# Performance work log

Hardware: AMD Instinct MI355X
Metric: run time of the kernel (lower is better)

## Reference

```python
import jax, jax.numpy as jnp
import numpy as np

B, IN, OUT, E = 4096, 256, 256, 16


def setup_inputs() -> dict:
    key = jax.random.key(0)
    k1, k2, k3, k4, k5, k6 = jax.random.split(key, 6)
    return {
        "input": jax.random.normal(k1, (B, IN), dtype=jnp.float32),
        "route_index": jax.random.randint(k2, (B,), 0, E),
        "weight": jax.random.normal(k3, (E, OUT * IN), dtype=jnp.float32) * 0.02,
        "weight_fact": jax.random.normal(k4, (1, OUT * IN), dtype=jnp.float32) * 0.02,
        "bias": jax.random.normal(k5, (E, OUT), dtype=jnp.float32) * 0.02,
        "bias_fact": jax.random.normal(k6, (1, OUT), dtype=jnp.float32) * 0.02,
    }


def reference(input, route_index, weight, weight_fact, bias, bias_fact):
    b = input.shape[0]
    # per-token expert weight gather + shared factorized weight
    expert_weight = (weight[route_index] + weight_fact).reshape(b, OUT, IN)
    expert_bias = bias[route_index] + bias_fact  # [b, OUT]
    # batched matvec
    out = jnp.einsum("bmn,bn->bm", expert_weight, input) + expert_bias
    return out
```

## Files before the change

### kernel.cpp

```cpp
#include <hip/hip_runtime.h>


#define B_TOK 4096
#define IN_F 256
#define OUT_F 256
#define NEXP 16
#define WEL (OUT_F * IN_F)
#define NSB 16

typedef __attribute__((ext_vector_type(8))) short bhalf8;
typedef __attribute__((ext_vector_type(4))) float v4f;

#define WSUM_OFF 0u
#define PART_OFF 2097152u

__device__ __forceinline__ unsigned short f2bf(float f) {
    unsigned u = __float_as_uint(f);
    u += 0x7FFFu + ((u >> 16) & 1u);
    return (unsigned short)(u >> 16);
}

__global__ __launch_bounds__(256) void k_prep(
    const int* __restrict__ ridx, const float* __restrict__ w,
    const float* __restrict__ wf, unsigned short* __restrict__ wsum,
    int* __restrict__ part) {
    int bid = blockIdx.x;
    int tid = threadIdx.x;
    if (bid < 512) {
        int id = (bid * 256 + tid) * 8;
        const float4 a0 = *(const float4*)(w + id);
        const float4 a1 = *(const float4*)(w + id + 4);
        int fo = id & (WEL - 1);
        const float4 f0 = *(const float4*)(wf + fo);
        const float4 f1 = *(const float4*)(wf + fo + 4);
        bhalf8 v;
        v[0] = (short)f2bf(a0.x + f0.x); v[1] = (short)f2bf(a0.y + f0.y);
        v[2] = (short)f2bf(a0.z + f0.z); v[3] = (short)f2bf(a0.w + f0.w);
        v[4] = (short)f2bf(a1.x + f1.x); v[5] = (short)f2bf(a1.y + f1.y);
        v[6] = (short)f2bf(a1.z + f1.z); v[7] = (short)f2bf(a1.w + f1.w);
        *(bhalf8*)(wsum + id) = v;
    } else {
        __shared__ int h[NEXP];
        if (tid < NEXP) h[tid] = 0;
        __syncthreads();
        int sb = bid - 512;
        atomicAdd(&h[ridx[sb * 256 + tid]], 1);
        __syncthreads();
        if (tid < NEXP) part[sb * NEXP + tid] = h[tid];
    }
}

__global__ __launch_bounds__(256) void k_gemm(
    const unsigned short* __restrict__ wsum, const float* __restrict__ x,
    const int* __restrict__ ridx, const int* __restrict__ part,
    const float* __restrict__ bias, const float* __restrict__ bf,
    float* __restrict__ out) {
    __shared__ int pfx[NSB + 1];
    __shared__ int wc[4];
    __shared__ int stk[16];

    int e = blockIdx.y;
    int j = blockIdx.x;
    int tid = threadIdx.x;

    __shared__ int pc[NSB];
    if (tid < NSB) pc[tid] = part[tid * NEXP + e];
    __syncthreads();
    if (tid == 0) {
        int a = 0;
        for (int sb = 0; sb < NSB; ++sb) { pfx[sb] = a; a += pc[sb]; }
        pfx[NSB] = a;
    }
    __syncthreads();
    int cnt = pfx[NSB];
    int start = j * 16;
    if (start >= cnt) return;
    int rem = cnt - start;
    int rows = rem < 16 ? rem : 16;
    int end = start + rows;

    int wave = tid >> 6;
    int lane = tid & 63;

    for (int sb = 0; sb < NSB; ++sb) {
        if (pfx[sb + 1] <= start || pfx[sb] >= end) continue;
        int tok = sb * 256 + tid;
        bool m = (ridx[tok] == e);
        unsigned long long mask = __ballot(m);
        if (lane == 0) wc[wave] = (int)__popcll(mask);
        __syncthreads();
        int wbase = 0;
        for (int wv = 0; wv < wave; ++wv) wbase += wc[wv];
        int rank = wbase + (int)__popcll(mask & ((1ull << lane) - 1ull));
        int slot = pfx[sb] + rank;
        if (m && slot >= start && slot < end) stk[slot - start] = tok;
        __syncthreads();
    }
    if (tid < 16 && tid >= rows) stk[tid] = stk[0];
    __syncthreads();

    int l15 = lane & 15;
    int quad = lane >> 4;

    const float* xrow = x + stk[l15] * IN_F + quad * 8;
    const unsigned short* wbase_p =
        wsum + e * WEL + (wave * 64 + l15) * IN_F + quad * 8;

    v4f acc[4];
    #pragma unroll
    for (int n = 0; n < 4; ++n) acc[n] = (v4f){0.f, 0.f, 0.f, 0.f};

    #pragma unroll
    for (int ks = 0; ks < 8; ++ks) {
        const float4 a0 = *(const float4*)(xrow + ks * 32);
        const float4 a1 = *(const float4*)(xrow + ks * 32 + 4);
        bhalf8 a;
        a[0] = (short)f2bf(a0.x); a[1] = (short)f2bf(a0.y);
        a[2] = (short)f2bf(a0.z); a[3] = (short)f2bf(a0.w);
        a[4] = (short)f2bf(a1.x); a[5] = (short)f2bf(a1.y);
        a[6] = (short)f2bf(a1.z); a[7] = (short)f2bf(a1.w);
        bhalf8 b0 = *(const bhalf8*)(wbase_p + 0 * 16 * IN_F + ks * 32);
        bhalf8 b1 = *(const bhalf8*)(wbase_p + 1 * 16 * IN_F + ks * 32);
        bhalf8 b2 = *(const bhalf8*)(wbase_p + 2 * 16 * IN_F + ks * 32);
        bhalf8 b3 = *(const bhalf8*)(wbase_p + 3 * 16 * IN_F + ks * 32);
        acc[0] = __builtin_amdgcn_mfma_f32_16x16x32_bf16(a, b0, acc[0], 0, 0, 0);
        acc[1] = __builtin_amdgcn_mfma_f32_16x16x32_bf16(a, b1, acc[1], 0, 0, 0);
        acc[2] = __builtin_amdgcn_mfma_f32_16x16x32_bf16(a, b2, acc[2], 0, 0, 0);
        acc[3] = __builtin_amdgcn_mfma_f32_16x16x32_bf16(a, b3, acc[3], 0, 0, 0);
    }

    #pragma unroll
    for (int n = 0; n < 4; ++n) {
        int m = wave * 64 + n * 16 + l15;
        float bb = bias[e * OUT_F + m] + bf[m];
        #pragma unroll
        for (int r = 0; r < 4; ++r) {
            int row = quad * 4 + r;
            if (row < rows) out[stk[row] * OUT_F + m] = acc[n][r] + bb;
        }
    }
}

extern "C" void kernel_launch(void* const* d_in, const int* in_sizes, int n_in,
                              void* d_out, int out_size, void* d_ws, size_t ws_size,
                              hipStream_t stream) {
    const float* x = (const float*)d_in[0];
    const int* ridx = (const int*)d_in[1];
    const float* w = (const float*)d_in[2];
    const float* wf = (const float*)d_in[3];
    const float* bias = (const float*)d_in[4];
    const float* bf = (const float*)d_in[5];
    float* out = (float*)d_out;
    char* ws = (char*)d_ws;

    unsigned short* wsum = (unsigned short*)(ws + WSUM_OFF);
    int* part = (int*)(ws + PART_OFF);

    k_prep<<<528, 256, 0, stream>>>(ridx, w, wf, wsum, part);
    k_gemm<<<dim3(32, NEXP), 256, 0, stream>>>(wsum, x, ridx, part, bias, bf, out);
}
```

Before: 83.70 us.

## Fuse weight folding and routing scan into a single gemm kernel

```diff
diff --git a/kernel.cpp b/kernel.cpp
--- a/kernel.cpp
+++ b/kernel.cpp
@@ -6,13 +6,9 @@
 #define OUT_F 256
 #define NEXP 16
 #define WEL (OUT_F * IN_F)
-#define NSB 16
 
 typedef __attribute__((ext_vector_type(8))) short bhalf8;
 typedef __attribute__((ext_vector_type(4))) float v4f;
-
-#define WSUM_OFF 0u
-#define PART_OFF 2097152u
 
 __device__ __forceinline__ unsigned short f2bf(float f) {
     unsigned u = __float_as_uint(f);
@@ -20,82 +16,56 @@
     return (unsigned short)(u >> 16);
 }
 
-__global__ __launch_bounds__(256) void k_prep(
-    const int* __restrict__ ridx, const float* __restrict__ w,
-    const float* __restrict__ wf, unsigned short* __restrict__ wsum,
-    int* __restrict__ part) {
-    int bid = blockIdx.x;
-    int tid = threadIdx.x;
-    if (bid < 512) {
-        int id = (bid * 256 + tid) * 8;
-        const float4 a0 = *(const float4*)(w + id);
-        const float4 a1 = *(const float4*)(w + id + 4);
-        int fo = id & (WEL - 1);
-        const float4 f0 = *(const float4*)(wf + fo);
-        const float4 f1 = *(const float4*)(wf + fo + 4);
-        bhalf8 v;
-        v[0] = (short)f2bf(a0.x + f0.x); v[1] = (short)f2bf(a0.y + f0.y);
-        v[2] = (short)f2bf(a0.z + f0.z); v[3] = (short)f2bf(a0.w + f0.w);
-        v[4] = (short)f2bf(a1.x + f1.x); v[5] = (short)f2bf(a1.y + f1.y);
-        v[6] = (short)f2bf(a1.z + f1.z); v[7] = (short)f2bf(a1.w + f1.w);
-        *(bhalf8*)(wsum + id) = v;
-    } else {
-        __shared__ int h[NEXP];
-        if (tid < NEXP) h[tid] = 0;
-        __syncthreads();
-        int sb = bid - 512;
-        atomicAdd(&h[ridx[sb * 256 + tid]], 1);
-        __syncthreads();
-        if (tid < NEXP) part[sb * NEXP + tid] = h[tid];
-    }
+__device__ __forceinline__ bhalf8 fold_bf8(const float* __restrict__ wp,
+                                           const float* __restrict__ fp) {
+    const float4 w0 = *(const float4*)(wp);
+    const float4 w1 = *(const float4*)(wp + 4);
+    const float4 f0 = *(const float4*)(fp);
+    const float4 f1 = *(const float4*)(fp + 4);
+    bhalf8 v;
+    v[0] = (short)f2bf(w0.x + f0.x); v[1] = (short)f2bf(w0.y + f0.y);
+    v[2] = (short)f2bf(w0.z + f0.z); v[3] = (short)f2bf(w0.w + f0.w);
+    v[4] = (short)f2bf(w1.x + f1.x); v[5] = (short)f2bf(w1.y + f1.y);
+    v[6] = (short)f2bf(w1.z + f1.z); v[7] = (short)f2bf(w1.w + f1.w);
+    return v;
 }
 
-__global__ __launch_bounds__(256) void k_gemm(
-    const unsigned short* __restrict__ wsum, const float* __restrict__ x,
-    const int* __restrict__ ridx, const int* __restrict__ part,
+__global__ __launch_bounds__(256) void k_fused(
+    const float* __restrict__ x, const int* __restrict__ ridx,
+    const float* __restrict__ w, const float* __restrict__ wf,
     const float* __restrict__ bias, const float* __restrict__ bf,
     float* __restrict__ out) {
-    __shared__ int pfx[NSB + 1];
     __shared__ int wc[4];
     __shared__ int stk[16];
 
     int e = blockIdx.y;
     int j = blockIdx.x;
     int tid = threadIdx.x;
-
-    __shared__ int pc[NSB];
-    if (tid < NSB) pc[tid] = part[tid * NEXP + e];
-    __syncthreads();
-    if (tid == 0) {
-        int a = 0;
-        for (int sb = 0; sb < NSB; ++sb) { pfx[sb] = a; a += pc[sb]; }
-        pfx[NSB] = a;
-    }
-    __syncthreads();
-    int cnt = pfx[NSB];
-    int start = j * 16;
-    if (start >= cnt) return;
-    int rem = cnt - start;
-    int rows = rem < 16 ? rem : 16;
-    int end = start + rows;
-
     int wave = tid >> 6;
     int lane = tid & 63;
+    int start = j * 16;
 
-    for (int sb = 0; sb < NSB; ++sb) {
-        if (pfx[sb + 1] <= start || pfx[sb] >= end) continue;
-        int tok = sb * 256 + tid;
+    int running = 0;
+    for (int c = 0; c < 16; ++c) {
+        int tok = c * 256 + tid;
         bool m = (ridx[tok] == e);
         unsigned long long mask = __ballot(m);
         if (lane == 0) wc[wave] = (int)__popcll(mask);
         __syncthreads();
-        int wbase = 0;
+        int wbase = running;
         for (int wv = 0; wv < wave; ++wv) wbase += wc[wv];
-        int rank = wbase + (int)__popcll(mask & ((1ull << lane) - 1ull));
-        int slot = pfx[sb] + rank;
-        if (m && slot >= start && slot < end) stk[slot - start] = tok;
+        if (m) {
+            int rank = wbase + (int)__popcll(mask & ((1ull << lane) - 1ull));
+            int slot = rank - start;
+            if (slot >= 0 && slot < 16) stk[slot] = tok;
+        }
+        running += wc[0] + wc[1] + wc[2] + wc[3];
         __syncthreads();
     }
+    int cnt = running;
+    if (start >= cnt) return;
+    int rem = cnt - start;
+    int rows = rem < 16 ? rem : 16;
     if (tid < 16 && tid >= rows) stk[tid] = stk[0];
     __syncthreads();
 
@@ -103,8 +73,9 @@
     int quad = lane >> 4;
 
     const float* xrow = x + stk[l15] * IN_F + quad * 8;
-    const unsigned short* wbase_p =
-        wsum + e * WEL + (wave * 64 + l15) * IN_F + quad * 8;
+    int mrow = wave * 64 + l15;
+    const float* wrow = w + e * WEL + mrow * IN_F + quad * 8;
+    const float* frow = wf + mrow * IN_F + quad * 8;
 
     v4f acc[4];
     #pragma unroll
@@ -119,14 +90,12 @@
         a[2] = (short)f2bf(a0.z); a[3] = (short)f2bf(a0.w);
         a[4] = (short)f2bf(a1.x); a[5] = (short)f2bf(a1.y);
         a[6] = (short)f2bf(a1.z); a[7] = (short)f2bf(a1.w);
-        bhalf8 b0 = *(const bhalf8*)(wbase_p + 0 * 16 * IN_F + ks * 32);
-        bhalf8 b1 = *(const bhalf8*)(wbase_p + 1 * 16 * IN_F + ks * 32);
-        bhalf8 b2 = *(const bhalf8*)(wbase_p + 2 * 16 * IN_F + ks * 32);
-        bhalf8 b3 = *(const bhalf8*)(wbase_p + 3 * 16 * IN_F + ks * 32);
-        acc[0] = __builtin_amdgcn_mfma_f32_16x16x32_bf16(a, b0, acc[0], 0, 0, 0);
-        acc[1] = __builtin_amdgcn_mfma_f32_16x16x32_bf16(a, b1, acc[1], 0, 0, 0);
-        acc[2] = __builtin_amdgcn_mfma_f32_16x16x32_bf16(a, b2, acc[2], 0, 0, 0);
-        acc[3] = __builtin_amdgcn_mfma_f32_16x16x32_bf16(a, b3, acc[3], 0, 0, 0);
+        #pragma unroll
+        for (int n = 0; n < 4; ++n) {
+            bhalf8 b = fold_bf8(wrow + n * 16 * IN_F + ks * 32,
+                                frow + n * 16 * IN_F + ks * 32);
+            acc[n] = __builtin_amdgcn_mfma_f32_16x16x32_bf16(a, b, acc[n], 0, 0, 0);
+        }
     }
 
     #pragma unroll
@@ -151,11 +120,6 @@
     const float* bias = (const float*)d_in[4];
     const float* bf = (const float*)d_in[5];
     float* out = (float*)d_out;
-    char* ws = (char*)d_ws;
 
-    unsigned short* wsum = (unsigned short*)(ws + WSUM_OFF);
-    int* part = (int*)(ws + PART_OFF);
-
-    k_prep<<<528, 256, 0, stream>>>(ridx, w, wf, wsum, part);
-    k_gemm<<<dim3(32, NEXP), 256, 0, stream>>>(wsum, x, ridx, part, bias, bf, out);
+    k_fused<<<dim3(32, NEXP), 256, 0, stream>>>(x, ridx, w, wf, bias, bf, out);
 }
```

After: 108.9 us. +30.1%, slower.

## Pre-convert input to bf16 and split output columns across more blocks

Applied to the files above, without the earlier changes.

```diff
diff --git a/kernel.cpp b/kernel.cpp
--- a/kernel.cpp
+++ b/kernel.cpp
@@ -12,7 +12,9 @@
 typedef __attribute__((ext_vector_type(4))) float v4f;
 
 #define WSUM_OFF 0u
-#define PART_OFF 2097152u
+#define XBF_OFF 2097152u
+#define BSUM_OFF 4194304u
+#define PART_OFF 4211712u
 
 __device__ __forceinline__ unsigned short f2bf(float f) {
     unsigned u = __float_as_uint(f);
@@ -21,9 +23,11 @@
 }
 
 __global__ __launch_bounds__(256) void k_prep(
-    const int* __restrict__ ridx, const float* __restrict__ w,
-    const float* __restrict__ wf, unsigned short* __restrict__ wsum,
-    int* __restrict__ part) {
+    const float* __restrict__ x, const int* __restrict__ ridx,
+    const float* __restrict__ w, const float* __restrict__ wf,
+    const float* __restrict__ bias, const float* __restrict__ bf,
+    unsigned short* __restrict__ wsum, unsigned short* __restrict__ xbf,
+    float* __restrict__ bsum, int* __restrict__ part) {
     int bid = blockIdx.x;
     int tid = threadIdx.x;
     if (bid < 512) {
@@ -39,31 +43,51 @@
         v[4] = (short)f2bf(a1.x + f1.x); v[5] = (short)f2bf(a1.y + f1.y);
         v[6] = (short)f2bf(a1.z + f1.z); v[7] = (short)f2bf(a1.w + f1.w);
         *(bhalf8*)(wsum + id) = v;
-    } else {
+    } else if (bid < 1024) {
+        int id = ((bid - 512) * 256 + tid) * 8;
+        const float4 a0 = *(const float4*)(x + id);
+        const float4 a1 = *(const float4*)(x + id + 4);
+        bhalf8 v;
+        v[0] = (short)f2bf(a0.x); v[1] = (short)f2bf(a0.y);
+        v[2] = (short)f2bf(a0.z); v[3] = (short)f2bf(a0.w);
+        v[4] = (short)f2bf(a1.x); v[5] = (short)f2bf(a1.y);
+        v[6] = (short)f2bf(a1.z); v[7] = (short)f2bf(a1.w);
+        *(bhalf8*)(xbf + id) = v;
+    } else if (bid < 1040) {
         __shared__ int h[NEXP];
         if (tid < NEXP) h[tid] = 0;
         __syncthreads();
-        int sb = bid - 512;
+        int sb = bid - 1024;
         atomicAdd(&h[ridx[sb * 256 + tid]], 1);
         __syncthreads();
         if (tid < NEXP) part[sb * NEXP + tid] = h[tid];
+    } else {
+        #pragma unroll
+        for (int q = 0; q < 4; ++q) {
+            int id = (q * 256 + tid) * 4;
+            const float4 a = *(const float4*)(bias + id);
+            const float4 f = *(const float4*)(bf + (id & (OUT_F - 1)));
+            float4 r;
+            r.x = a.x + f.x; r.y = a.y + f.y; r.z = a.z + f.z; r.w = a.w + f.w;
+            *(float4*)(bsum + id) = r;
+        }
     }
 }
 
 __global__ __launch_bounds__(256) void k_gemm(
-    const unsigned short* __restrict__ wsum, const float* __restrict__ x,
-    const int* __restrict__ ridx, const int* __restrict__ part,
-    const float* __restrict__ bias, const float* __restrict__ bf,
-    float* __restrict__ out) {
+    const unsigned short* __restrict__ wsum, const unsigned short* __restrict__ xbf,
+    const float* __restrict__ bsum, const int* __restrict__ part,
+    const int* __restrict__ ridx, float* __restrict__ out) {
+    __shared__ int pc[NSB];
     __shared__ int pfx[NSB + 1];
     __shared__ int wc[4];
     __shared__ int stk[16];
 
-    int e = blockIdx.y;
+    int e = blockIdx.z;
     int j = blockIdx.x;
+    int g = blockIdx.y;
     int tid = threadIdx.x;
 
-    __shared__ int pc[NSB];
     if (tid < NSB) pc[tid] = part[tid * NEXP + e];
     __syncthreads();
     if (tid == 0) {
@@ -101,43 +125,28 @@
 
     int l15 = lane & 15;
     int quad = lane >> 4;
+    int n0 = g * 64 + wave * 16;
 
-    const float* xrow = x + stk[l15] * IN_F + quad * 8;
-    const unsigned short* wbase_p =
-        wsum + e * WEL + (wave * 64 + l15) * IN_F + quad * 8;
+    const unsigned short* xr = xbf + stk[l15] * IN_F + quad * 8;
+    const unsigned short* wr = wsum + e * WEL + (n0 + l15) * IN_F + quad * 8;
 
-    v4f acc[4];
-    #pragma unroll
-    for (int n = 0; n < 4; ++n) acc[n] = (v4f){0.f, 0.f, 0.f, 0.f};
-
+    bhalf8 areg[8], breg[8];
     #pragma unroll
     for (int ks = 0; ks < 8; ++ks) {
-        const float4 a0 = *(const float4*)(xrow + ks * 32);
-        const float4 a1 = *(const float4*)(xrow + ks * 32 + 4);
-        bhalf8 a;
-        a[0] = (short)f2bf(a0.x); a[1] = (short)f2bf(a0.y);
-        a[2] = (short)f2bf(a0.z); a[3] = (short)f2bf(a0.w);
-        a[4] = (short)f2bf(a1.x); a[5] = (short)f2bf(a1.y);
-        a[6] = (short)f2bf(a1.z); a[7] = (short)f2bf(a1.w);
-        bhalf8 b0 = *(const bhalf8*)(wbase_p + 0 * 16 * IN_F + ks * 32);
-        bhalf8 b1 = *(const bhalf8*)(wbase_p + 1 * 16 * IN_F + ks * 32);
-        bhalf8 b2 = *(const bhalf8*)(wbase_p + 2 * 16 * IN_F + ks * 32);
-        bhalf8 b3 = *(const bhalf8*)(wbase_p + 3 * 16 * IN_F + ks * 32);
-        acc[0] = __builtin_amdgcn_mfma_f32_16x16x32_bf16(a, b0, acc[0], 0, 0, 0);
-        acc[1] = __builtin_amdgcn_mfma_f32_16x16x32_bf16(a, b1, acc[1], 0, 0, 0);
-        acc[2] = __builtin_amdgcn_mfma_f32_16x16x32_bf16(a, b2, acc[2], 0, 0, 0);
-        acc[3] = __builtin_amdgcn_mfma_f32_16x16x32_bf16(a, b3, acc[3], 0, 0, 0);
+        areg[ks] = *(const bhalf8*)(xr + ks * 32);
+        breg[ks] = *(const bhalf8*)(wr + ks * 32);
     }
+    v4f acc = (v4f){0.f, 0.f, 0.f, 0.f};
+    #pragma unroll
+    for (int ks = 0; ks < 8; ++ks)
+        acc = __builtin_amdgcn_mfma_f32_16x16x32_bf16(areg[ks], breg[ks], acc, 0, 0, 0);
 
+    int m = n0 + l15;
+    float bb = bsum[e * OUT_F + m];
     #pragma unroll
-    for (int n = 0; n < 4; ++n) {
-        int m = wave * 64 + n * 16 + l15;
-        float bb = bias[e * OUT_F + m] + bf[m];
-        #pragma unroll
-        for (int r = 0; r < 4; ++r) {
-            int row = quad * 4 + r;
-            if (row < rows) out[stk[row] * OUT_F + m] = acc[n][r] + bb;
-        }
+    for (int r = 0; r < 4; ++r) {
+        int row = quad * 4 + r;
+        if (row < rows) out[stk[row] * OUT_F + m] = acc[r] + bb;
     }
 }
 
@@ -154,8 +163,10 @@
     char* ws = (char*)d_ws;
 
     unsigned short* wsum = (unsigned short*)(ws + WSUM_OFF);
+    unsigned short* xbf = (unsigned short*)(ws + XBF_OFF);
+    float* bsum = (float*)(ws + BSUM_OFF);
     int* part = (int*)(ws + PART_OFF);
 
-    k_prep<<<528, 256, 0, stream>>>(ridx, w, wf, wsum, part);
-    k_gemm<<<dim3(32, NEXP), 256, 0, stream>>>(wsum, x, ridx, part, bias, bf, out);
+    k_prep<<<1041, 256, 0, stream>>>(x, ridx, w, wf, bias, bf, wsum, xbf, bsum, part);
+    k_gemm<<<dim3(32, 4, NEXP), 256, 0, stream>>>(wsum, xbf, bsum, part, ridx, out);
 }
```

Result: slower. 87.32 us (+4.3%).
